# Kernel optimization log

Measured on AMD Instinct MI355X. Metric: run time of the kernel, lower is better.

Reference implementation:

```python
import math
import jax, jax.numpy as jnp
import numpy as np

B, Q, K = 1, 2048, 2048
CQ = CK = CV = 128
H, CH = 8, 32
HD = H * CH  # 256


def setup_inputs() -> dict:
    key = jax.random.key(0)
    ks = jax.random.split(key, 12)
    s = 0.02
    return {
        "q_x": jax.random.normal(ks[0], (B, Q, CQ), jnp.float32),
        "kv_x": jax.random.normal(ks[1], (B, K, CK), jnp.float32),
        "bias": jax.random.normal(ks[2], (B, 1, Q, K), jnp.float32),
        "distance": jax.random.uniform(ks[3], (B, Q, K, H), jnp.float32),
        "Wq": jax.random.normal(ks[4], (CQ, HD), jnp.float32) * s,
        "Wk": jax.random.normal(ks[5], (CK, HD), jnp.float32) * s,
        "Wv": jax.random.normal(ks[6], (CV, HD), jnp.float32) * s,
        "Wg": jax.random.normal(ks[7], (CQ, HD), jnp.float32) * s,
        "bg": jnp.zeros((HD,), jnp.float32),
        "Wo": jax.random.normal(ks[8], (HD, CQ), jnp.float32) * s,
        "bo": jnp.zeros((CQ,), jnp.float32),
    }


def reference(q_x, kv_x, bias, distance, Wq, Wk, Wv, Wg, bg, Wo, bo):
    # Projections -> [B, S, H, CH]
    q = (q_x @ Wq).reshape(B, Q, H, CH) / math.sqrt(CH)
    k = (kv_x @ Wk).reshape(B, K, H, CH)
    v = (kv_x @ Wv).reshape(B, K, H, CH)
    # Scores [B, H, Q, K]
    a = jnp.einsum("bqhc,bkhc->bhqk", q, k)
    a = a + bias
    # mha_permu=True: distance [B,Q,K,H] -> [B,H,Q,K]; rel_dis_pair_bias='add'
    a = a + jnp.transpose(distance, (0, 3, 1, 2))
    a = jax.nn.softmax(a, axis=-1)
    o = jnp.einsum("bhqk,bkhc->bqhc", a, v)  # [B, Q, H, CH]
    # Gating
    g = jax.nn.sigmoid(q_x @ Wg + bg).reshape(B, Q, H, CH)
    o = o * g
    o = o.reshape(B, Q, HD)
    return o @ Wo + bo
```

## Files before the change

### kernel.cpp

```cpp
#include <hip/hip_runtime.h>
#include <hip/hip_bf16.h>

#define Qn 2048
#define Kn 2048
#define Cin 128
#define Hn 8
#define CHn 32
#define HDn 256
#define NSPLIT 8
#define KP 68

typedef __attribute__((ext_vector_type(8))) short short8;
typedef __attribute__((ext_vector_type(4))) float f32x4;

static __device__ __forceinline__ unsigned short f2bf(float f) {
    unsigned int u = __float_as_uint(f);
    u += 0x7fffu + ((u >> 16) & 1u);
    return (unsigned short)(u >> 16);
}

__global__ __launch_bounds__(256) void proj_kernel(
    const float* __restrict__ qx, const float* __restrict__ kvx,
    const float* __restrict__ Wq, const float* __restrict__ Wk,
    const float* __restrict__ Wv, const float* __restrict__ Wg,
    const float* __restrict__ bg,
    unsigned short* __restrict__ qb, unsigned short* __restrict__ kb,
    unsigned short* __restrict__ vtb, float* __restrict__ gb)
{
    const int mat = blockIdx.y;
    const int r0 = blockIdx.x * 8;
    const int j = threadIdx.x;
    const float* A = (mat == 0 || mat == 3) ? qx : kvx;
    const float* W = (mat == 0) ? Wq : (mat == 1) ? Wk : (mat == 2) ? Wv : Wg;
    const float* Ar = A + r0 * Cin;
    float acc[8] = {0.f, 0.f, 0.f, 0.f, 0.f, 0.f, 0.f, 0.f};
    for (int c = 0; c < Cin; ++c) {
        const float w = W[c * HDn + j];
        #pragma unroll
        for (int i = 0; i < 8; ++i)
            acc[i] = fmaf(Ar[i * Cin + c], w, acc[i]);
    }
    if (mat == 0) {
        const float s = 0.17677669529663687f;
        #pragma unroll
        for (int i = 0; i < 8; ++i)
            qb[(r0 + i) * HDn + j] = f2bf(acc[i] * s);
    } else if (mat == 1) {
        #pragma unroll
        for (int i = 0; i < 8; ++i)
            kb[(r0 + i) * HDn + j] = f2bf(acc[i]);
    } else if (mat == 2) {
        unsigned short tmp[8];
        #pragma unroll
        for (int i = 0; i < 8; ++i) tmp[i] = f2bf(acc[i]);
        *(short8*)(vtb + (size_t)j * Kn + r0) = *(short8*)tmp;
    } else {
        const float b = bg[j];
        #pragma unroll
        for (int i = 0; i < 8; ++i)
            gb[(r0 + i) * HDn + j] = 1.f / (1.f + __expf(-(acc[i] + b)));
    }
}

__global__ __launch_bounds__(512, 6) void attn_kernel(
    const unsigned short* __restrict__ qb, const unsigned short* __restrict__ kb,
    const unsigned short* __restrict__ vtb,
    const float* __restrict__ bias, const float* __restrict__ dist,
    float* __restrict__ opart, float* __restrict__ lpart)
{
    __shared__ unsigned short ps[Hn][16][72];
    __shared__ _Float16 dbl[Hn * 16 * KP];

    const int bx = blockIdx.x;
    const int qt = bx >> 3;
    const int sp = bx & 7;
    const int q0 = qt * 16;
    const int k00 = sp * 256;
    const int t = threadIdx.x;
    const int h = t >> 6;
    const int l = t & 63;
    const int g = l >> 4;
    const int n = l & 15;

    const int sk = (t >> 1) & 63;
    const int shg = t & 1;
    const int sqb = t >> 7;

    const short8 qf = *(const short8*)(qb + (q0 + n) * HDn + h * CHn + g * 8);

    f32x4 o0 = {0.f, 0.f, 0.f, 0.f};
    f32x4 o1 = {0.f, 0.f, 0.f, 0.f};
    float lacc[4] = {0.f, 0.f, 0.f, 0.f};
    unsigned short* psh = &ps[h][0][0];
    const f32x4 z = {0.f, 0.f, 0.f, 0.f};

    f32x4 dv[4];
    float bv[4];
    #pragma unroll
    for (int i = 0; i < 4; ++i) {
        const int qi = q0 + sqb + 4 * i;
        dv[i] = *(const f32x4*)(dist + ((size_t)qi * Kn + k00 + sk) * Hn + 4 * shg);
        bv[i] = bias[(size_t)qi * Kn + k00 + sk];
    }

    for (int kt = 0; kt < 4; ++kt) {
        const int k0 = k00 + kt * 64;
        __syncthreads();
        #pragma unroll
        for (int i = 0; i < 4; ++i) {
            const int qi = sqb + 4 * i;
            #pragma unroll
            for (int j = 0; j < 4; ++j)
                dbl[((shg * 4 + j) * 16 + qi) * KP + sk] = (_Float16)(dv[i][j] + bv[i]);
        }
        __syncthreads();
        if (kt < 3) {
            #pragma unroll
            for (int i = 0; i < 4; ++i) {
                const int qi = q0 + sqb + 4 * i;
                dv[i] = *(const f32x4*)(dist + ((size_t)qi * Kn + k0 + 64 + sk) * Hn + 4 * shg);
                bv[i] = bias[(size_t)qi * Kn + k0 + 64 + sk];
            }
        }
        f32x4 sf[4];
        #pragma unroll
        for (int kkg = 0; kkg < 4; ++kkg) {
            const short8 kf = *(const short8*)(kb + (k0 + kkg * 16 + n) * HDn + h * CHn + g * 8);
            sf[kkg] = __builtin_amdgcn_mfma_f32_16x16x32_bf16(qf, kf, z, 0, 0, 0);
        }
        const _Float16* dbh = dbl + h * 16 * KP;
        #pragma unroll
        for (int kkg = 0; kkg < 4; ++kkg) {
            #pragma unroll
            for (int r = 0; r < 4; ++r) {
                const float db = (float)dbh[(g * 4 + r) * KP + kkg * 16 + n];
                const float p = __expf(sf[kkg][r] + db);
                sf[kkg][r] = p;
                lacc[r] += p;
            }
        }
        #pragma unroll
        for (int kkg = 0; kkg < 4; ++kkg) {
            #pragma unroll
            for (int r = 0; r < 4; ++r)
                psh[(g * 4 + r) * 72 + kkg * 16 + n] = f2bf(sf[kkg][r]);
        }
        #pragma unroll
        for (int chunk = 0; chunk < 2; ++chunk) {
            const short8 pf = *(const short8*)(psh + n * 72 + chunk * 32 + g * 8);
            const short8 vf0 = *(const short8*)(vtb + (h * CHn + n) * Kn + k0 + chunk * 32 + g * 8);
            o0 = __builtin_amdgcn_mfma_f32_16x16x32_bf16(pf, vf0, o0, 0, 0, 0);
            const short8 vf1 = *(const short8*)(vtb + (h * CHn + 16 + n) * Kn + k0 + chunk * 32 + g * 8);
            o1 = __builtin_amdgcn_mfma_f32_16x16x32_bf16(pf, vf1, o1, 0, 0, 0);
        }
    }
    float* op = opart + (size_t)sp * (Qn * HDn);
    #pragma unroll
    for (int r = 0; r < 4; ++r) {
        const int qg = q0 + g * 4 + r;
        op[qg * HDn + h * CHn + n] = o0[r];
        op[qg * HDn + h * CHn + 16 + n] = o1[r];
        float v = lacc[r];
        v += __shfl_xor(v, 1);
        v += __shfl_xor(v, 2);
        v += __shfl_xor(v, 4);
        v += __shfl_xor(v, 8);
        lacc[r] = v;
    }
    if (n == 0) {
        float* lp = lpart + (size_t)sp * (Qn * Hn);
        #pragma unroll
        for (int r = 0; r < 4; ++r)
            lp[(q0 + g * 4 + r) * Hn + h] = lacc[r];
    }
}

__global__ __launch_bounds__(256) void mergeout_kernel(
    const float* __restrict__ opart, const float* __restrict__ lpart,
    const float* __restrict__ gb, const float* __restrict__ Wo,
    const float* __restrict__ bo, float* __restrict__ out)
{
    __shared__ float olds[HDn];
    __shared__ float red[4][128];
    const int q = blockIdx.x;
    const int t = threadIdx.x;
    const int h = t >> 5;
    float s = 0.f;
    #pragma unroll
    for (int sp = 0; sp < NSPLIT; ++sp)
        s += opart[(size_t)sp * (Qn * HDn) + q * HDn + t];
    float lt = 0.f;
    #pragma unroll
    for (int sp = 0; sp < NSPLIT; ++sp)
        lt += lpart[(size_t)sp * (Qn * Hn) + q * Hn + h];
    olds[t] = (s / lt) * gb[q * HDn + t];
    __syncthreads();
    const int p = t & 63;
    const int seg = t >> 6;
    float a0 = 0.f, a1 = 0.f;
    for (int c = seg * 64; c < seg * 64 + 64; ++c) {
        const float ov = olds[c];
        const float2 w = *(const float2*)(Wo + c * Cin + 2 * p);
        a0 = fmaf(ov, w.x, a0);
        a1 = fmaf(ov, w.y, a1);
    }
    red[seg][2 * p] = a0;
    red[seg][2 * p + 1] = a1;
    __syncthreads();
    if (t < 128)
        out[q * Cin + t] = red[0][t] + red[1][t] + red[2][t] + red[3][t] + bo[t];
}

extern "C" void kernel_launch(void* const* d_in, const int* in_sizes, int n_in,
                              void* d_out, int out_size, void* d_ws, size_t ws_size,
                              hipStream_t stream)
{
    const float* qx   = (const float*)d_in[0];
    const float* kvx  = (const float*)d_in[1];
    const float* bias = (const float*)d_in[2];
    const float* dist = (const float*)d_in[3];
    const float* Wq   = (const float*)d_in[4];
    const float* Wk   = (const float*)d_in[5];
    const float* Wv   = (const float*)d_in[6];
    const float* Wg   = (const float*)d_in[7];
    const float* bg   = (const float*)d_in[8];
    const float* Wo   = (const float*)d_in[9];
    const float* bo   = (const float*)d_in[10];
    float* out = (float*)d_out;

    char* w = (char*)d_ws;
    unsigned short* qb  = (unsigned short*)(w);
    unsigned short* kb  = (unsigned short*)(w + (1ull << 20));
    unsigned short* vtb = (unsigned short*)(w + (2ull << 20));
    float* gb    = (float*)(w + (3ull << 20));
    float* opart = (float*)(w + (5ull << 20));
    float* lpart = (float*)(w + (21ull << 20));

    proj_kernel<<<dim3(Qn / 8, 4), 256, 0, stream>>>(qx, kvx, Wq, Wk, Wv, Wg, bg, qb, kb, vtb, gb);
    attn_kernel<<<dim3(128 * NSPLIT), 512, 0, stream>>>(qb, kb, vtb, bias, dist, opart, lpart);
    mergeout_kernel<<<dim3(Qn), 256, 0, stream>>>(opart, lpart, gb, Wo, bo, out);
}
```

Measured before the change: 281.9 us.

## Double-buffer the attention bias tile in LDS and drop a per-iteration barrier

The shared fp16 tile holding bias plus distance now has two buffers. The next tile is written into the alternate buffer after the PV MFMAs, which removes the second __syncthreads from each key-tile iteration. The K fragment loads are hoisted ahead of the distance and bias prefetch, and the staging thread mapping is changed so that lanes walk consecutive keys, which should cut LDS write bank conflicts. The cost is roughly double the LDS footprint for this tile, which may lower how many blocks fit per CU, and less contiguous global loads for the distance tensor.

```diff
diff --git a/kernel.cpp b/kernel.cpp
--- a/kernel.cpp
+++ b/kernel.cpp
@@ -69,7 +69,7 @@
     float* __restrict__ opart, float* __restrict__ lpart)
 {
     __shared__ unsigned short ps[Hn][16][72];
-    __shared__ _Float16 dbl[Hn * 16 * KP];
+    __shared__ _Float16 dbl[2][Hn * 16 * KP];
 
     const int bx = blockIdx.x;
     const int qt = bx >> 3;
@@ -82,9 +82,9 @@
     const int g = l >> 4;
     const int n = l & 15;
 
-    const int sk = (t >> 1) & 63;
-    const int shg = t & 1;
-    const int sqb = t >> 7;
+    const int sk = t & 63;
+    const int sqb = (t >> 6) & 3;
+    const int shg = t >> 8;
 
     const short8 qf = *(const short8*)(qb + (q0 + n) * HDn + h * CHn + g * 8);
 
@@ -102,18 +102,21 @@
         dv[i] = *(const f32x4*)(dist + ((size_t)qi * Kn + k00 + sk) * Hn + 4 * shg);
         bv[i] = bias[(size_t)qi * Kn + k00 + sk];
     }
+    #pragma unroll
+    for (int i = 0; i < 4; ++i) {
+        #pragma unroll
+        for (int j = 0; j < 4; ++j)
+            dbl[0][((shg * 4 + j) * 16 + sqb + 4 * i) * KP + sk] = (_Float16)(dv[i][j] + bv[i]);
+    }
+    int buf = 0;
 
     for (int kt = 0; kt < 4; ++kt) {
         const int k0 = k00 + kt * 64;
         __syncthreads();
-        #pragma unroll
-        for (int i = 0; i < 4; ++i) {
-            const int qi = sqb + 4 * i;
-            #pragma unroll
-            for (int j = 0; j < 4; ++j)
-                dbl[((shg * 4 + j) * 16 + qi) * KP + sk] = (_Float16)(dv[i][j] + bv[i]);
-        }
-        __syncthreads();
+        short8 kfr[4];
+        #pragma unroll
+        for (int kkg = 0; kkg < 4; ++kkg)
+            kfr[kkg] = *(const short8*)(kb + (k0 + kkg * 16 + n) * HDn + h * CHn + g * 8);
         if (kt < 3) {
             #pragma unroll
             for (int i = 0; i < 4; ++i) {
@@ -124,11 +127,9 @@
         }
         f32x4 sf[4];
         #pragma unroll
-        for (int kkg = 0; kkg < 4; ++kkg) {
-            const short8 kf = *(const short8*)(kb + (k0 + kkg * 16 + n) * HDn + h * CHn + g * 8);
-            sf[kkg] = __builtin_amdgcn_mfma_f32_16x16x32_bf16(qf, kf, z, 0, 0, 0);
-        }
-        const _Float16* dbh = dbl + h * 16 * KP;
+        for (int kkg = 0; kkg < 4; ++kkg)
+            sf[kkg] = __builtin_amdgcn_mfma_f32_16x16x32_bf16(qf, kfr[kkg], z, 0, 0, 0);
+        const _Float16* dbh = dbl[buf] + h * 16 * KP;
         #pragma unroll
         for (int kkg = 0; kkg < 4; ++kkg) {
             #pragma unroll
@@ -153,6 +154,15 @@
             const short8 vf1 = *(const short8*)(vtb + (h * CHn + 16 + n) * Kn + k0 + chunk * 32 + g * 8);
             o1 = __builtin_amdgcn_mfma_f32_16x16x32_bf16(pf, vf1, o1, 0, 0, 0);
         }
+        if (kt < 3) {
+            #pragma unroll
+            for (int i = 0; i < 4; ++i) {
+                #pragma unroll
+                for (int j = 0; j < 4; ++j)
+                    dbl[buf ^ 1][((shg * 4 + j) * 16 + sqb + 4 * i) * KP + sk] = (_Float16)(dv[i][j] + bv[i]);
+            }
+        }
+        buf ^= 1;
     }
     float* op = opart + (size_t)sp * (Qn * HDn);
     #pragma unroll
```

After: 295.7 us. 1.05x slower.

## Split attention blocks by head group and double key splits

Applied to the files above, without the earlier changes.

Each attention block now handles 4 heads (256 threads) instead of 8, and the key dimension is split 16 ways instead of 8. The grid grows from 1024 to 4096 smaller blocks, each doing 2 key tiles, to raise occupancy and balance load across CUs. In exchange, the bias reads are duplicated across the two head-group blocks, the register prefetch pipeline is shorter, and the partial-output buffer the merge kernel must read and sum doubles in size.

```diff
diff --git a/kernel.cpp b/kernel.cpp
--- a/kernel.cpp
+++ b/kernel.cpp
@@ -7,7 +7,7 @@
 #define Hn 8
 #define CHn 32
 #define HDn 256
-#define NSPLIT 8
+#define NSPLIT 16
 #define KP 68
 
 typedef __attribute__((ext_vector_type(8))) short short8;
@@ -62,63 +62,64 @@
     }
 }
 
-__global__ __launch_bounds__(512, 6) void attn_kernel(
+__global__ __launch_bounds__(256, 6) void attn_kernel(
     const unsigned short* __restrict__ qb, const unsigned short* __restrict__ kb,
     const unsigned short* __restrict__ vtb,
     const float* __restrict__ bias, const float* __restrict__ dist,
     float* __restrict__ opart, float* __restrict__ lpart)
 {
-    __shared__ unsigned short ps[Hn][16][72];
-    __shared__ _Float16 dbl[Hn * 16 * KP];
+    __shared__ unsigned short ps[4][16][72];
+    __shared__ _Float16 dbl[4 * 16 * KP];
 
     const int bx = blockIdx.x;
-    const int qt = bx >> 3;
-    const int sp = bx & 7;
+    const int hg = bx & 1;
+    const int sp = (bx >> 1) & (NSPLIT - 1);
+    const int qt = bx >> 5;
     const int q0 = qt * 16;
-    const int k00 = sp * 256;
+    const int k00 = sp * (Kn / NSPLIT);
+    const int hbase = hg * 4;
     const int t = threadIdx.x;
-    const int h = t >> 6;
+    const int w = t >> 6;
+    const int h = hbase + w;
     const int l = t & 63;
     const int g = l >> 4;
     const int n = l & 15;
 
-    const int sk = (t >> 1) & 63;
-    const int shg = t & 1;
-    const int sqb = t >> 7;
+    const int sk = t & 63;
+    const int sq = t >> 6;
 
     const short8 qf = *(const short8*)(qb + (q0 + n) * HDn + h * CHn + g * 8);
 
     f32x4 o0 = {0.f, 0.f, 0.f, 0.f};
     f32x4 o1 = {0.f, 0.f, 0.f, 0.f};
     float lacc[4] = {0.f, 0.f, 0.f, 0.f};
-    unsigned short* psh = &ps[h][0][0];
+    unsigned short* psh = &ps[w][0][0];
     const f32x4 z = {0.f, 0.f, 0.f, 0.f};
 
     f32x4 dv[4];
     float bv[4];
     #pragma unroll
     for (int i = 0; i < 4; ++i) {
-        const int qi = q0 + sqb + 4 * i;
-        dv[i] = *(const f32x4*)(dist + ((size_t)qi * Kn + k00 + sk) * Hn + 4 * shg);
+        const int qi = q0 + sq + 4 * i;
+        dv[i] = *(const f32x4*)(dist + ((size_t)qi * Kn + k00 + sk) * Hn + 4 * hg);
         bv[i] = bias[(size_t)qi * Kn + k00 + sk];
     }
 
-    for (int kt = 0; kt < 4; ++kt) {
+    for (int kt = 0; kt < Kn / NSPLIT / 64; ++kt) {
         const int k0 = k00 + kt * 64;
         __syncthreads();
         #pragma unroll
         for (int i = 0; i < 4; ++i) {
-            const int qi = sqb + 4 * i;
             #pragma unroll
             for (int j = 0; j < 4; ++j)
-                dbl[((shg * 4 + j) * 16 + qi) * KP + sk] = (_Float16)(dv[i][j] + bv[i]);
+                dbl[(j * 16 + sq + 4 * i) * KP + sk] = (_Float16)(dv[i][j] + bv[i]);
         }
         __syncthreads();
-        if (kt < 3) {
+        if (kt < 1) {
             #pragma unroll
             for (int i = 0; i < 4; ++i) {
-                const int qi = q0 + sqb + 4 * i;
-                dv[i] = *(const f32x4*)(dist + ((size_t)qi * Kn + k0 + 64 + sk) * Hn + 4 * shg);
+                const int qi = q0 + sq + 4 * i;
+                dv[i] = *(const f32x4*)(dist + ((size_t)qi * Kn + k0 + 64 + sk) * Hn + 4 * hg);
                 bv[i] = bias[(size_t)qi * Kn + k0 + 64 + sk];
             }
         }
@@ -128,7 +129,7 @@
             const short8 kf = *(const short8*)(kb + (k0 + kkg * 16 + n) * HDn + h * CHn + g * 8);
             sf[kkg] = __builtin_amdgcn_mfma_f32_16x16x32_bf16(qf, kf, z, 0, 0, 0);
         }
-        const _Float16* dbh = dbl + h * 16 * KP;
+        const _Float16* dbh = dbl + w * 16 * KP;
         #pragma unroll
         for (int kkg = 0; kkg < 4; ++kkg) {
             #pragma unroll
@@ -234,9 +235,9 @@
     unsigned short* vtb = (unsigned short*)(w + (2ull << 20));
     float* gb    = (float*)(w + (3ull << 20));
     float* opart = (float*)(w + (5ull << 20));
-    float* lpart = (float*)(w + (21ull << 20));
+    float* lpart = (float*)(w + (37ull << 20));
 
     proj_kernel<<<dim3(Qn / 8, 4), 256, 0, stream>>>(qx, kvx, Wq, Wk, Wv, Wg, bg, qb, kb, vtb, gb);
-    attn_kernel<<<dim3(128 * NSPLIT), 512, 0, stream>>>(qb, kb, vtb, bias, dist, opart, lpart);
+    attn_kernel<<<dim3(128 * NSPLIT * 2), 256, 0, stream>>>(qb, kb, vtb, bias, dist, opart, lpart);
     mergeout_kernel<<<dim3(Qn), 256, 0, stream>>>(opart, lpart, gb, Wo, bo, out);
 }
```

Result: slower. 295.8 us (+4.9%).
